# Optimization experiments

Measured on AMD Instinct MI355X. Metric: run time of the kernel, lower is better.

## Reference

```python
import jax, jax.numpy as jnp
import numpy as np

NO_FEATURES = 512
NO_HEADS = 8
HEAD_DIM = NO_FEATURES // NO_HEADS


def setup_inputs() -> dict:
    key = jax.random.key(0)
    ks = jax.random.split(key, 10)
    B, S, D = 4, 2048, NO_FEATURES
    s = 1.0 / np.sqrt(D)
    return {
        "x": jax.random.normal(ks[0], (B, S, D), dtype=jnp.float32),
        "ln_gamma": jnp.ones((D,), jnp.float32),
        "ln_beta": jnp.zeros((D,), jnp.float32),
        "Wq": jax.random.uniform(ks[1], (D, D), jnp.float32, -s, s),
        "bq": jax.random.uniform(ks[2], (D,), jnp.float32, -s, s),
        "Wk": jax.random.uniform(ks[3], (D, D), jnp.float32, -s, s),
        "bk": jax.random.uniform(ks[4], (D,), jnp.float32, -s, s),
        "Wv": jax.random.uniform(ks[5], (D, D), jnp.float32, -s, s),
        "bv": jax.random.uniform(ks[6], (D,), jnp.float32, -s, s),
        "Wo": jax.random.uniform(ks[7], (D, D), jnp.float32, -s, s),
        "bo": jax.random.uniform(ks[8], (D,), jnp.float32, -s, s),
    }


def reference(x, ln_gamma, ln_beta, Wq, bq, Wk, bk, Wv, bv, Wo, bo):
    B, S, D = x.shape
    H, Dh = NO_HEADS, D // NO_HEADS
    # Pre-LayerNorm (eps = 1e-5, torch default)
    mu = jnp.mean(x, axis=-1, keepdims=True)
    var = jnp.mean(jnp.square(x - mu), axis=-1, keepdims=True)
    xn = (x - mu) * jax.lax.rsqrt(var + 1e-5) * ln_gamma + ln_beta
    # QKV projections (torch Linear: x @ W.T + b)
    q = (xn @ Wq.T + bq).reshape(B, S, H, Dh).transpose(0, 2, 1, 3)
    k = (xn @ Wk.T + bk).reshape(B, S, H, Dh).transpose(0, 2, 1, 3)
    v = (xn @ Wv.T + bv).reshape(B, S, H, Dh).transpose(0, 2, 1, 3)
    scale = Dh ** -0.5
    scores = jnp.einsum("bhqd,bhkd->bhqk", q, k) * scale  # [B,H,S,S]
    attn = jax.nn.softmax(scores, axis=-1)
    # dropout is identity in eval mode
    out = jnp.einsum("bhqk,bhkd->bhqd", attn, v)
    out = out.transpose(0, 2, 1, 3).reshape(B, S, D)
    return out @ Wo.T + bo
```

## Files before the change

kernel.cpp:

```cpp
#include <hip/hip_runtime.h>
#include <cstdint>
#include <cstddef>

#define NB 4
#define NS 2048
#define ND 512
#define NH 8
#define DH 64
#define MTOK (NB*NS)

typedef __bf16 bf16x8 __attribute__((ext_vector_type(8)));
typedef float f32x4 __attribute__((ext_vector_type(4)));
typedef float f32x16 __attribute__((ext_vector_type(16)));
typedef unsigned int u32x4 __attribute__((ext_vector_type(4)));
typedef unsigned short ushort_t;
typedef unsigned int uint_t;

__device__ __forceinline__ unsigned short f2bf(float f) {
  unsigned int u = __builtin_bit_cast(unsigned int, f);
  return (unsigned short)((u + 0x7fffu + ((u >> 16) & 1u)) >> 16);
}

__device__ __forceinline__ uint_t cvtpk(float lo, float hi) {
  uint_t r;
  asm("v_cvt_pk_bf16_f32 %0, %1, %2" : "=v"(r) : "v"(lo), "v"(hi));
  return r;
}

__device__ __forceinline__ void pswap(uint_t &a, uint_t &b) {
  asm("v_permlane32_swap_b32 %0, %1" : "+v"(a), "+v"(b));
}

__device__ __forceinline__ void gload_lds16(const void* g, void* l) {
  __builtin_amdgcn_global_load_lds(
      (const __attribute__((address_space(1))) unsigned int*)g,
      (__attribute__((address_space(3))) unsigned int*)l,
      16, 0, 0);
}

__device__ __forceinline__ bf16x8 ld8(const ushort_t* p) { return *(const bf16x8*)p; }

__global__ __launch_bounds__(256) void ln_conv(
    const float* __restrict__ x, const float* __restrict__ gamma,
    const float* __restrict__ beta, ushort_t* __restrict__ xn,
    const float* __restrict__ Wq, const float* __restrict__ Wk,
    const float* __restrict__ Wv, const float* __restrict__ Wo,
    ushort_t* __restrict__ wqkv, ushort_t* __restrict__ wob)
{
  if (blockIdx.x >= 2048) {
    const int t = (blockIdx.x - 2048)*256 + threadIdx.x;
    const int i = t*8;
    const float* src; ushort_t* dst;
    if (i < 1536*512) {
      const int n = i >> 9, c = i & 511;
      const float* W = (n < 512) ? Wq : (n < 1024) ? Wk : Wv;
      src = W + ((size_t)(n & 511) << 9) + c;
      dst = wqkv + i;
    } else {
      const int jj = i - 1536*512;
      src = Wo + jj; dst = wob + jj;
    }
    float4 a = ((const float4*)src)[0], b = ((const float4*)src)[1];
    uint4 o;
    o.x = (uint_t)f2bf(a.x) | ((uint_t)f2bf(a.y)<<16);
    o.y = (uint_t)f2bf(a.z) | ((uint_t)f2bf(a.w)<<16);
    o.z = (uint_t)f2bf(b.x) | ((uint_t)f2bf(b.y)<<16);
    o.w = (uint_t)f2bf(b.z) | ((uint_t)f2bf(b.w)<<16);
    *(uint4*)dst = o;
    return;
  }
  const int row  = blockIdx.x * 4 + (threadIdx.x >> 6);
  const int lane = threadIdx.x & 63;
  const float4* xr = (const float4*)(x + (size_t)row * ND);
  float4 a = xr[lane*2], b = xr[lane*2+1];
  float v[8] = {a.x,a.y,a.z,a.w,b.x,b.y,b.z,b.w};
  float s = 0.f, s2 = 0.f;
#pragma unroll
  for (int j = 0; j < 8; ++j) { s += v[j]; s2 += v[j]*v[j]; }
#pragma unroll
  for (int mk = 1; mk < 64; mk <<= 1) { s += __shfl_xor(s, mk); s2 += __shfl_xor(s2, mk); }
  const float mu = s * (1.0f/ND);
  const float rs = rsqrtf(s2*(1.0f/ND) - mu*mu + 1e-5f);
  const float4* g4 = (const float4*)gamma;
  const float4* b4 = (const float4*)beta;
  float4 g0 = g4[lane*2], g1 = g4[lane*2+1];
  float4 e0 = b4[lane*2], e1 = b4[lane*2+1];
  float gv[8] = {g0.x,g0.y,g0.z,g0.w,g1.x,g1.y,g1.z,g1.w};
  float ev[8] = {e0.x,e0.y,e0.z,e0.w,e1.x,e1.y,e1.z,e1.w};
  unsigned short o[8];
#pragma unroll
  for (int j = 0; j < 8; ++j) o[j] = f2bf((v[j]-mu)*rs*gv[j] + ev[j]);
  uint4 ov;
  ov.x = (uint_t)o[0] | ((uint_t)o[1]<<16);
  ov.y = (uint_t)o[2] | ((uint_t)o[3]<<16);
  ov.z = (uint_t)o[4] | ((uint_t)o[5]<<16);
  ov.w = (uint_t)o[6] | ((uint_t)o[7]<<16);
  ((uint4*)(xn + (size_t)row*ND))[lane] = ov;
}

template<int EPI>
__global__ __launch_bounds__(256, 2) void gemm_bt(
    const ushort_t* __restrict__ A, const ushort_t* __restrict__ Bw, int Kd,
    const float* __restrict__ bq, const float* __restrict__ bk, const float* __restrict__ bv,
    ushort_t* __restrict__ qa, ushort_t* __restrict__ ka, ushort_t* __restrict__ vta,
    const float* __restrict__ bo, float* __restrict__ outp)
{
  __shared__ ushort_t lA[2][128*32];
  __shared__ ushort_t lB[2][128*32];
  const int tid = threadIdx.x;
  const int wave = tid >> 6, lane = tid & 63;
  const int m0 = blockIdx.y * 128, n0 = blockIdx.x * 128;
  const int wr = (wave >> 1) * 64, wc = (wave & 1) * 64;

  f32x4 acc[4][4] = {};

  const ushort_t* aS = A  + (size_t)(m0 + tid/4) * Kd + (tid & 3) * 8;
  const ushort_t* bS = Bw + (size_t)(n0 + tid/4) * Kd + (tid & 3) * 8;
  const size_t half = (size_t)64 * Kd;
  const int NT = Kd / 32;

#define STAGE(BUF, K0)                                            \
  gload_lds16(aS + (K0),        lA[BUF] + wave*512);              \
  gload_lds16(aS + half + (K0), lA[BUF] + 2048 + wave*512);       \
  gload_lds16(bS + (K0),        lB[BUF] + wave*512);              \
  gload_lds16(bS + half + (K0), lB[BUF] + 2048 + wave*512);

  STAGE(0, 0);
  int cur = 0;
  for (int t = 0; t < NT; ++t) {
    if (t + 1 < NT) {
      STAGE(cur ^ 1, (t + 1) * 32);
      asm volatile("s_waitcnt vmcnt(4)" ::: "memory");
    } else {
      asm volatile("s_waitcnt vmcnt(0)" ::: "memory");
    }
    __builtin_amdgcn_s_barrier();
    asm volatile("" ::: "memory");
    bf16x8 af[4], bfr[4];
#pragma unroll
    for (int i = 0; i < 4; ++i)
      af[i] = *(const bf16x8*)(lA[cur] + (wr + i*16 + (lane&15))*32 + (lane>>4)*8);
#pragma unroll
    for (int j = 0; j < 4; ++j)
      bfr[j] = *(const bf16x8*)(lB[cur] + (wc + j*16 + (lane&15))*32 + (lane>>4)*8);
#pragma unroll
    for (int i = 0; i < 4; ++i)
#pragma unroll
      for (int j = 0; j < 4; ++j)
        acc[i][j] = __builtin_amdgcn_mfma_f32_16x16x32_bf16(af[i], bfr[j], acc[i][j], 0, 0, 0);
    asm volatile("s_waitcnt lgkmcnt(0)" ::: "memory");
    __builtin_amdgcn_s_barrier();
    asm volatile("" ::: "memory");
    cur ^= 1;
  }
#undef STAGE

  if (EPI == 0) {
    const float QSCALE = 0.18033688011112042f;
#pragma unroll
    for (int j = 0; j < 4; ++j) {
      const int n = n0 + wc + j*16 + (lane & 15);
      const int which = n >> 9;
      const int nn = n & 511;
      const int h = nn >> 6, d = nn & 63;
      const float bb = (which == 0) ? bq[nn] : (which == 1) ? bk[nn] : bv[nn];
#pragma unroll
      for (int i = 0; i < 4; ++i)
#pragma unroll
        for (int r = 0; r < 4; ++r) {
          const int mm = m0 + wr + i*16 + 4*(lane>>4) + r;
          const int b = mm >> 11, s = mm & 2047;
          const int bh = b*NH + h;
          const float av = acc[i][j][r] + bb;
          if (which == 0) {
            qa[(((size_t)bh*64 + (s>>5))*4 + (d>>4))*512
               + (((d>>3)&1)*32 + (s&31))*8 + (d&7)] = f2bf(av * QSCALE);
          } else if (which == 1) {
            ka[(((size_t)bh*64 + (s>>5))*4 + (d>>4))*512
               + (((d>>3)&1)*32 + (s&31))*8 + (d&7)] = f2bf(av);
          } else {
            vta[(((size_t)bh*128 + (s>>4))*2 + (d>>5))*512
               + (((s>>3)&1)*32 + (d&31))*8 + (s&7)] = f2bf(av);
          }
        }
    }
  } else {
#pragma unroll
    for (int j = 0; j < 4; ++j) {
      const int n = n0 + wc + j*16 + (lane & 15);
      const float bb = bo[n];
#pragma unroll
      for (int i = 0; i < 4; ++i)
#pragma unroll
        for (int r = 0; r < 4; ++r) {
          const int m = m0 + wr + i*16 + 4*(lane>>4) + r;
          outp[(size_t)m*ND + n] = acc[i][j][r] + bb;
        }
    }
  }
}

__global__ __launch_bounds__(256) void attn_kernel(
    const ushort_t* __restrict__ qfv, const ushort_t* __restrict__ kfv,
    const ushort_t* __restrict__ vfv, ushort_t* __restrict__ ao)
{
  const int blk  = blockIdx.x;
  const int bh   = (blk & 7) | ((blk >> 7) << 3);
  const int qblk = (blk >> 3) & 15;
  const int w    = threadIdx.x >> 6;
  const int lane = threadIdx.x & 63;
  const int lo5 = lane & 31, hi = lane >> 5;
  const int qt = qblk*4 + w;

  const ushort_t* qb = qfv + (((size_t)bh*64 + qt)*4)*512 + lane*8;
  bf16x8 qf[4];
#pragma unroll
  for (int s = 0; s < 4; ++s) qf[s] = ld8(qb + s*512);

  const ushort_t* kpA = kfv + ((size_t)bh*256)*512 + lane*8;
  const ushort_t* kpB = kpA + 2048;
  const ushort_t* vpA = vfv + ((size_t)bh*256)*512 + lane*8;
  const ushort_t* vpB = vpA + 2048;

  const uint_t one2 = 0x3F803F80u;
  const bf16x8 ones = __builtin_bit_cast(bf16x8, (u32x4){one2, one2, one2, one2});

  f32x16 o0 = {}, o1 = {}, ol = {};

  bf16x8 kf0[4], kf1[4];
#pragma unroll
  for (int s = 0; s < 4; ++s) {
    kf0[s] = ld8(kpA + s*512);
    kf1[s] = ld8(kpB + s*512);
  }
  kpA += 4096; kpB += 4096;

  for (int t = 0; t < 32; ++t) {
    bf16x8 vf0[4], vf1[4];
    vf0[0] = ld8(vpA);        vf1[0] = ld8(vpA + 512);
    vf0[1] = ld8(vpA + 1024); vf1[1] = ld8(vpA + 1536);
    vf0[2] = ld8(vpB);        vf1[2] = ld8(vpB + 512);
    vf0[3] = ld8(vpB + 1024); vf1[3] = ld8(vpB + 1536);
    vpA += 4096; vpB += 4096;
    f32x16 s0 = {}, s1 = {};
#pragma unroll
    for (int s = 0; s < 4; ++s) {
      s0 = __builtin_amdgcn_mfma_f32_32x32x16_bf16(kf0[s], qf[s], s0, 0, 0, 0);
      s1 = __builtin_amdgcn_mfma_f32_32x32x16_bf16(kf1[s], qf[s], s1, 0, 0, 0);
    }
    if (t < 31) {
#pragma unroll
      for (int s = 0; s < 4; ++s) {
        kf0[s] = ld8(kpA + s*512);
        kf1[s] = ld8(kpB + s*512);
      }
      kpA += 4096; kpB += 4096;
    }
#pragma unroll
    for (int r = 0; r < 16; ++r) s0[r] = __builtin_amdgcn_exp2f(s0[r]);
#pragma unroll
    for (int r = 0; r < 16; ++r) s1[r] = __builtin_amdgcn_exp2f(s1[r]);
    bf16x8 pf[4];
    {
      uint_t a, b, c, d;
      a = cvtpk(s0[0],  s0[1]);  b = cvtpk(s0[4],  s0[5]);  pswap(a, b);
      c = cvtpk(s0[2],  s0[3]);  d = cvtpk(s0[6],  s0[7]);  pswap(c, d);
      pf[0] = __builtin_bit_cast(bf16x8, (u32x4){a, c, b, d});
      a = cvtpk(s0[8],  s0[9]);  b = cvtpk(s0[12], s0[13]); pswap(a, b);
      c = cvtpk(s0[10], s0[11]); d = cvtpk(s0[14], s0[15]); pswap(c, d);
      pf[1] = __builtin_bit_cast(bf16x8, (u32x4){a, c, b, d});
      a = cvtpk(s1[0],  s1[1]);  b = cvtpk(s1[4],  s1[5]);  pswap(a, b);
      c = cvtpk(s1[2],  s1[3]);  d = cvtpk(s1[6],  s1[7]);  pswap(c, d);
      pf[2] = __builtin_bit_cast(bf16x8, (u32x4){a, c, b, d});
      a = cvtpk(s1[8],  s1[9]);  b = cvtpk(s1[12], s1[13]); pswap(a, b);
      c = cvtpk(s1[10], s1[11]); d = cvtpk(s1[14], s1[15]); pswap(c, d);
      pf[3] = __builtin_bit_cast(bf16x8, (u32x4){a, c, b, d});
    }
#pragma unroll
    for (int ks = 0; ks < 4; ++ks)
      ol = __builtin_amdgcn_mfma_f32_32x32x16_bf16(ones, pf[ks], ol, 0, 0, 0);
#pragma unroll
    for (int ks = 0; ks < 4; ++ks) {
      o0 = __builtin_amdgcn_mfma_f32_32x32x16_bf16(vf0[ks], pf[ks], o0, 0, 0, 0);
      o1 = __builtin_amdgcn_mfma_f32_32x32x16_bf16(vf1[ks], pf[ks], o1, 0, 0, 0);
    }
  }

  const float rl = __builtin_amdgcn_rcpf(ol[0]);
  const int b = bh >> 3, h = bh & 7;
  const int srow = qt*32 + lo5;
  ushort_t* ob = ao + ((size_t)(b*NS + srow))*ND + h*DH;
#pragma unroll
  for (int dt = 0; dt < 2; ++dt) {
    f32x16& oo = dt ? o1 : o0;
#pragma unroll
    for (int r = 0; r < 16; r += 2) {
      const int d = (r & 3) + 8*(r >> 2) + 4*hi + dt*32;
      *(uint_t*)(ob + d) = cvtpk(oo[r]*rl, oo[r+1]*rl);
    }
  }
}

extern "C" void kernel_launch(void* const* d_in, const int* in_sizes, int n_in,
                              void* d_out, int out_size, void* d_ws, size_t ws_size,
                              hipStream_t stream)
{
  const float* x  = (const float*)d_in[0];
  const float* g  = (const float*)d_in[1];
  const float* be = (const float*)d_in[2];
  const float* Wq = (const float*)d_in[3];
  const float* bq = (const float*)d_in[4];
  const float* Wk = (const float*)d_in[5];
  const float* bk = (const float*)d_in[6];
  const float* Wv = (const float*)d_in[7];
  const float* bv = (const float*)d_in[8];
  const float* Wo = (const float*)d_in[9];
  const float* bo = (const float*)d_in[10];
  float* out = (float*)d_out;

  char* w = (char*)d_ws;
  ushort_t* xn   = (ushort_t*)w; w += (size_t)MTOK*ND*2;
  ushort_t* wqkv = (ushort_t*)w; w += (size_t)1536*512*2;
  ushort_t* wob  = (ushort_t*)w; w += (size_t)512*512*2;
  ushort_t* qa   = (ushort_t*)w; w += (size_t)MTOK*ND*2;
  ushort_t* ka   = (ushort_t*)w; w += (size_t)MTOK*ND*2;
  ushort_t* vta  = (ushort_t*)w; w += (size_t)MTOK*ND*2;
  ushort_t* ao   = (ushort_t*)w; w += (size_t)MTOK*ND*2;

  ln_conv<<<2560, 256, 0, stream>>>(x, g, be, xn, Wq, Wk, Wv, Wo, wqkv, wob);
  gemm_bt<0><<<dim3(12, 64), 256, 0, stream>>>(xn, wqkv, ND,
      bq, bk, bv, qa, ka, vta, nullptr, nullptr);
  attn_kernel<<<512, 256, 0, stream>>>(qa, ka, vta, ao);
  gemm_bt<1><<<dim3(4, 64), 256, 0, stream>>>(ao, wob, ND,
      nullptr, nullptr, nullptr, nullptr, nullptr, nullptr, bo, out);
}
```

Before: 104.4 us.

## Split attention key range in two and combine partial outputs in a new kernel

Splits each attention work item along the key dimension into two halves, doubling the grid from 512 to 1024 blocks. Each half writes unnormalized fp32 partial outputs and row sums, and a new combine kernel adds them, normalizes and writes the bf16 attention output. This targets low occupancy or tail effects from only 512 blocks on a large GPU. The cost is extra fp32 global traffic and one more kernel launch, and the output buffer and the Q buffer are reused as scratch. The exp is done without a max subtraction in both halves, so the sums stay consistent.

```diff
diff --git a/kernel.cpp b/kernel.cpp
--- a/kernel.cpp
+++ b/kernel.cpp
@@ -8,6 +8,7 @@
 #define NH 8
 #define DH 64
 #define MTOK (NB*NS)
+#define NROW (NB*NH*NS)
 
 typedef __bf16 bf16x8 __attribute__((ext_vector_type(8)));
 typedef float f32x4 __attribute__((ext_vector_type(4)));
@@ -202,13 +203,15 @@
 
 __global__ __launch_bounds__(256) void attn_kernel(
     const ushort_t* __restrict__ qfv, const ushort_t* __restrict__ kfv,
-    const ushort_t* __restrict__ vfv, ushort_t* __restrict__ ao)
-{
-  const int blk  = blockIdx.x;
-  const int bh   = (blk & 7) | ((blk >> 7) << 3);
-  const int qblk = (blk >> 3) & 15;
-  const int w    = threadIdx.x >> 6;
-  const int lane = threadIdx.x & 63;
+    const ushort_t* __restrict__ vfv, float* __restrict__ op0,
+    float* __restrict__ op1, float* __restrict__ lsum)
+{
+  const int blk   = blockIdx.x;
+  const int bh    = (blk & 7) | ((blk >> 8) << 3);
+  const int qblk  = (blk >> 3) & 15;
+  const int split = (blk >> 7) & 1;
+  const int w     = threadIdx.x >> 6;
+  const int lane  = threadIdx.x & 63;
   const int lo5 = lane & 31, hi = lane >> 5;
   const int qt = qblk*4 + w;
 
@@ -217,9 +220,9 @@
 #pragma unroll
   for (int s = 0; s < 4; ++s) qf[s] = ld8(qb + s*512);
 
-  const ushort_t* kpA = kfv + ((size_t)bh*256)*512 + lane*8;
+  const ushort_t* kpA = kfv + ((size_t)bh*256 + split*128)*512 + lane*8;
   const ushort_t* kpB = kpA + 2048;
-  const ushort_t* vpA = vfv + ((size_t)bh*256)*512 + lane*8;
+  const ushort_t* vpA = vfv + ((size_t)bh*256 + split*128)*512 + lane*8;
   const ushort_t* vpB = vpA + 2048;
 
   const uint_t one2 = 0x3F803F80u;
@@ -235,7 +238,7 @@
   }
   kpA += 4096; kpB += 4096;
 
-  for (int t = 0; t < 32; ++t) {
+  for (int t = 0; t < 16; ++t) {
     bf16x8 vf0[4], vf1[4];
     vf0[0] = ld8(vpA);        vf1[0] = ld8(vpA + 512);
     vf0[1] = ld8(vpA + 1024); vf1[1] = ld8(vpA + 1536);
@@ -248,7 +251,7 @@
       s0 = __builtin_amdgcn_mfma_f32_32x32x16_bf16(kf0[s], qf[s], s0, 0, 0, 0);
       s1 = __builtin_amdgcn_mfma_f32_32x32x16_bf16(kf1[s], qf[s], s1, 0, 0, 0);
     }
-    if (t < 31) {
+    if (t < 15) {
 #pragma unroll
       for (int s = 0; s < 4; ++s) {
         kf0[s] = ld8(kpA + s*512);
@@ -286,19 +289,39 @@
     }
   }
 
-  const float rl = __builtin_amdgcn_rcpf(ol[0]);
-  const int b = bh >> 3, h = bh & 7;
-  const int srow = qt*32 + lo5;
-  ushort_t* ob = ao + ((size_t)(b*NS + srow))*ND + h*DH;
+  const int row = bh*NS + qt*32 + lo5;
+  float* ob = (split ? op1 : op0) + (size_t)row * DH;
 #pragma unroll
   for (int dt = 0; dt < 2; ++dt) {
     f32x16& oo = dt ? o1 : o0;
 #pragma unroll
     for (int r = 0; r < 16; r += 2) {
       const int d = (r & 3) + 8*(r >> 2) + 4*hi + dt*32;
-      *(uint_t*)(ob + d) = cvtpk(oo[r]*rl, oo[r+1]*rl);
-    }
-  }
+      float2 v2; v2.x = oo[r]; v2.y = oo[r+1];
+      *(float2*)(ob + d) = v2;
+    }
+  }
+  if (hi == 0) lsum[(size_t)split*NROW + row] = ol[0];
+}
+
+__global__ __launch_bounds__(256) void combine_kernel(
+    const float* __restrict__ op0, const float* __restrict__ op1,
+    const float* __restrict__ lsum, ushort_t* __restrict__ ao)
+{
+  const int t = blockIdx.x*256 + threadIdx.x;
+  const int row = t >> 3, d8 = (t & 7) * 8;
+  const float rl = 1.0f / (lsum[row] + lsum[NROW + row]);
+  const float4 a0 = *(const float4*)(op0 + (size_t)row*DH + d8);
+  const float4 a1 = *(const float4*)(op0 + (size_t)row*DH + d8 + 4);
+  const float4 b0 = *(const float4*)(op1 + (size_t)row*DH + d8);
+  const float4 b1 = *(const float4*)(op1 + (size_t)row*DH + d8 + 4);
+  u32x4 o;
+  o[0] = cvtpk((a0.x+b0.x)*rl, (a0.y+b0.y)*rl);
+  o[1] = cvtpk((a0.z+b0.z)*rl, (a0.w+b0.w)*rl);
+  o[2] = cvtpk((a1.x+b1.x)*rl, (a1.y+b1.y)*rl);
+  o[3] = cvtpk((a1.z+b1.z)*rl, (a1.w+b1.w)*rl);
+  const int bh = row >> 11, s = row & 2047, bb = bh >> 3, h = bh & 7;
+  *(u32x4*)(ao + ((size_t)(bb*NS + s))*ND + h*DH + d8) = o;
 }
 
 extern "C" void kernel_launch(void* const* d_in, const int* in_sizes, int n_in,
@@ -325,12 +348,16 @@
   ushort_t* qa   = (ushort_t*)w; w += (size_t)MTOK*ND*2;
   ushort_t* ka   = (ushort_t*)w; w += (size_t)MTOK*ND*2;
   ushort_t* vta  = (ushort_t*)w; w += (size_t)MTOK*ND*2;
-  ushort_t* ao   = (ushort_t*)w; w += (size_t)MTOK*ND*2;
+  float*    lsum = (float*)w;    w += (size_t)2*NROW*4;
+  float*    op1  = (float*)w;    w += (size_t)NROW*DH*4;
+  float* op0 = (float*)d_out;
+  ushort_t* ao = qa;
 
   ln_conv<<<2560, 256, 0, stream>>>(x, g, be, xn, Wq, Wk, Wv, Wo, wqkv, wob);
   gemm_bt<0><<<dim3(12, 64), 256, 0, stream>>>(xn, wqkv, ND,
       bq, bk, bv, qa, ka, vta, nullptr, nullptr);
-  attn_kernel<<<512, 256, 0, stream>>>(qa, ka, vta, ao);
+  attn_kernel<<<1024, 256, 0, stream>>>(qa, ka, vta, op0, op1, lsum);
+  combine_kernel<<<NROW*8/256, 256, 0, stream>>>(op0, op1, lsum, ao);
   gemm_bt<1><<<dim3(4, 64), 256, 0, stream>>>(ao, wob, ND,
       nullptr, nullptr, nullptr, nullptr, nullptr, nullptr, bo, out);
 }
```

Measured after the change: 111.2 us. 6.5% more time.

## Remap GEMM blocks across XCDs, rotate attention KV start, sum softmax denominator in VALU

Applied to the files above, without the earlier changes.

The GEMM launches become 1D grids whose block index is remapped so that consecutive tiles land on the same XCD. This is meant to improve L2 reuse of A and B tiles. In attention, half the blocks begin their KV sweep at the midpoint of the sequence, spreading simultaneous reads across different K/V regions. The row-sum MFMA against a ones matrix is replaced by VALU accumulation of the exp values plus a cross-half shuffle, which removes four MFMAs per iteration at the cost of extra adds.

```diff
diff --git a/kernel.cpp b/kernel.cpp
--- a/kernel.cpp
+++ b/kernel.cpp
@@ -98,7 +98,7 @@
   ((uint4*)(xn + (size_t)row*ND))[lane] = ov;
 }
 
-template<int EPI>
+template<int EPI, int NTN>
 __global__ __launch_bounds__(256, 2) void gemm_bt(
     const ushort_t* __restrict__ A, const ushort_t* __restrict__ Bw, int Kd,
     const float* __restrict__ bq, const float* __restrict__ bk, const float* __restrict__ bv,
@@ -109,7 +109,8 @@
   __shared__ ushort_t lB[2][128*32];
   const int tid = threadIdx.x;
   const int wave = tid >> 6, lane = tid & 63;
-  const int m0 = blockIdx.y * 128, n0 = blockIdx.x * 128;
+  const int wg = (blockIdx.x & 7) * (gridDim.x >> 3) + (blockIdx.x >> 3);
+  const int m0 = (wg / NTN) * 128, n0 = (wg % NTN) * 128;
   const int wr = (wave >> 1) * 64, wc = (wave & 1) * 64;
 
   f32x4 acc[4][4] = {};
@@ -207,6 +208,7 @@
   const int blk  = blockIdx.x;
   const int bh   = (blk & 7) | ((blk >> 7) << 3);
   const int qblk = (blk >> 3) & 15;
+  const int ro   = (blk >> 8) & 1 ? 16 : 0;
   const int w    = threadIdx.x >> 6;
   const int lane = threadIdx.x & 63;
   const int lo5 = lane & 31, hi = lane >> 5;
@@ -217,31 +219,27 @@
 #pragma unroll
   for (int s = 0; s < 4; ++s) qf[s] = ld8(qb + s*512);
 
-  const ushort_t* kpA = kfv + ((size_t)bh*256)*512 + lane*8;
-  const ushort_t* kpB = kpA + 2048;
-  const ushort_t* vpA = vfv + ((size_t)bh*256)*512 + lane*8;
-  const ushort_t* vpB = vpA + 2048;
-
-  const uint_t one2 = 0x3F803F80u;
-  const bf16x8 ones = __builtin_bit_cast(bf16x8, (u32x4){one2, one2, one2, one2});
-
-  f32x16 o0 = {}, o1 = {}, ol = {};
+  const ushort_t* kb = kfv + ((size_t)bh*256)*512 + lane*8;
+  const ushort_t* vb = vfv + ((size_t)bh*256)*512 + lane*8;
+
+  f32x16 o0 = {}, o1 = {};
+  float l0 = 0.f, l1 = 0.f, l2 = 0.f, l3 = 0.f;
 
   bf16x8 kf0[4], kf1[4];
 #pragma unroll
   for (int s = 0; s < 4; ++s) {
-    kf0[s] = ld8(kpA + s*512);
-    kf1[s] = ld8(kpB + s*512);
-  }
-  kpA += 4096; kpB += 4096;
+    kf0[s] = ld8(kb + ((size_t)(ro*8) + s)*512);
+    kf1[s] = ld8(kb + ((size_t)(ro*8) + 4 + s)*512);
+  }
 
   for (int t = 0; t < 32; ++t) {
+    const int idx = (t + ro) & 31;
     bf16x8 vf0[4], vf1[4];
-    vf0[0] = ld8(vpA);        vf1[0] = ld8(vpA + 512);
-    vf0[1] = ld8(vpA + 1024); vf1[1] = ld8(vpA + 1536);
-    vf0[2] = ld8(vpB);        vf1[2] = ld8(vpB + 512);
-    vf0[3] = ld8(vpB + 1024); vf1[3] = ld8(vpB + 1536);
-    vpA += 4096; vpB += 4096;
+#pragma unroll
+    for (int ks = 0; ks < 4; ++ks) {
+      vf0[ks] = ld8(vb + ((size_t)(idx*4 + ks)*2    )*512);
+      vf1[ks] = ld8(vb + ((size_t)(idx*4 + ks)*2 + 1)*512);
+    }
     f32x16 s0 = {}, s1 = {};
 #pragma unroll
     for (int s = 0; s < 4; ++s) {
@@ -249,17 +247,27 @@
       s1 = __builtin_amdgcn_mfma_f32_32x32x16_bf16(kf1[s], qf[s], s1, 0, 0, 0);
     }
     if (t < 31) {
+      const int nidx = (t + 1 + ro) & 31;
 #pragma unroll
       for (int s = 0; s < 4; ++s) {
-        kf0[s] = ld8(kpA + s*512);
-        kf1[s] = ld8(kpB + s*512);
+        kf0[s] = ld8(kb + ((size_t)(nidx*8) + s)*512);
+        kf1[s] = ld8(kb + ((size_t)(nidx*8) + 4 + s)*512);
       }
-      kpA += 4096; kpB += 4096;
-    }
-#pragma unroll
-    for (int r = 0; r < 16; ++r) s0[r] = __builtin_amdgcn_exp2f(s0[r]);
-#pragma unroll
-    for (int r = 0; r < 16; ++r) s1[r] = __builtin_amdgcn_exp2f(s1[r]);
+    }
+#pragma unroll
+    for (int r = 0; r < 16; r += 4) {
+      s0[r]   = __builtin_amdgcn_exp2f(s0[r]);   l0 += s0[r];
+      s0[r+1] = __builtin_amdgcn_exp2f(s0[r+1]); l1 += s0[r+1];
+      s0[r+2] = __builtin_amdgcn_exp2f(s0[r+2]); l2 += s0[r+2];
+      s0[r+3] = __builtin_amdgcn_exp2f(s0[r+3]); l3 += s0[r+3];
+    }
+#pragma unroll
+    for (int r = 0; r < 16; r += 4) {
+      s1[r]   = __builtin_amdgcn_exp2f(s1[r]);   l0 += s1[r];
+      s1[r+1] = __builtin_amdgcn_exp2f(s1[r+1]); l1 += s1[r+1];
+      s1[r+2] = __builtin_amdgcn_exp2f(s1[r+2]); l2 += s1[r+2];
+      s1[r+3] = __builtin_amdgcn_exp2f(s1[r+3]); l3 += s1[r+3];
+    }
     bf16x8 pf[4];
     {
       uint_t a, b, c, d;
@@ -277,16 +285,15 @@
       pf[3] = __builtin_bit_cast(bf16x8, (u32x4){a, c, b, d});
     }
 #pragma unroll
-    for (int ks = 0; ks < 4; ++ks)
-      ol = __builtin_amdgcn_mfma_f32_32x32x16_bf16(ones, pf[ks], ol, 0, 0, 0);
-#pragma unroll
     for (int ks = 0; ks < 4; ++ks) {
       o0 = __builtin_amdgcn_mfma_f32_32x32x16_bf16(vf0[ks], pf[ks], o0, 0, 0, 0);
       o1 = __builtin_amdgcn_mfma_f32_32x32x16_bf16(vf1[ks], pf[ks], o1, 0, 0, 0);
     }
   }
 
-  const float rl = __builtin_amdgcn_rcpf(ol[0]);
+  float l = (l0 + l1) + (l2 + l3);
+  l += __shfl_xor(l, 32);
+  const float rl = __builtin_amdgcn_rcpf(l);
   const int b = bh >> 3, h = bh & 7;
   const int srow = qt*32 + lo5;
   ushort_t* ob = ao + ((size_t)(b*NS + srow))*ND + h*DH;
@@ -328,9 +335,9 @@
   ushort_t* ao   = (ushort_t*)w; w += (size_t)MTOK*ND*2;
 
   ln_conv<<<2560, 256, 0, stream>>>(x, g, be, xn, Wq, Wk, Wv, Wo, wqkv, wob);
-  gemm_bt<0><<<dim3(12, 64), 256, 0, stream>>>(xn, wqkv, ND,
+  gemm_bt<0, 12><<<768, 256, 0, stream>>>(xn, wqkv, ND,
       bq, bk, bv, qa, ka, vta, nullptr, nullptr);
   attn_kernel<<<512, 256, 0, stream>>>(qa, ka, vta, ao);
-  gemm_bt<1><<<dim3(4, 64), 256, 0, stream>>>(ao, wob, ND,
+  gemm_bt<1, 4><<<256, 256, 0, stream>>>(ao, wob, ND,
       nullptr, nullptr, nullptr, nullptr, nullptr, nullptr, bo, out);
 }
```

Measured after the change: 93.22 us (median of 2 runs). 1.12x faster.
